# Kernel tuning notes

Measured on AMD Instinct MI355X. Metric: run time of the kernel, lower is better.

Reference implementation:

```python
import jax, jax.numpy as jnp
import numpy as np
import math

EPS = 1e-12  # F.normalize default eps

def _l2_normalize(x):
    n = jnp.sqrt(jnp.sum(x * x, axis=-1, keepdims=True))
    return x / jnp.maximum(n, EPS)

def setup_inputs() -> dict:
    key = jax.random.key(0)
    k1, k2 = jax.random.split(key)
    B, F, C = 16384, 1024, 1000
    features = jax.random.normal(k1, (B, F), dtype=jnp.float32)
    prototypes = jax.random.normal(k2, (C, F), dtype=jnp.float32)
    distance_scale = jnp.ones((1,), dtype=jnp.float32)
    temperature = jnp.ones((1,), dtype=jnp.float32)
    return {"features": features, "prototypes": prototypes,
            "distance_scale": distance_scale, "temperature": temperature}

def reference(features, prototypes, distance_scale, temperature):
    # L2-normalize both sides (F.normalize, p=2, eps=1e-12)
    f = _l2_normalize(features)      # [B, F]
    p = _l2_normalize(prototypes)    # [C, F]
    # Pairwise Euclidean distance. For unit vectors ||f-p||^2 = 2 - 2 f.p,
    # clamped at 0 for numerical safety; then / sqrt(2).
    sim = jnp.einsum('bf,cf->bc', f, p)                  # [B, C]
    sq = jnp.maximum(2.0 - 2.0 * sim, 0.0)
    distances = jnp.sqrt(sq) / jnp.float32(math.sqrt(2.0))
    iso = jnp.abs(distance_scale) * distances            # [B, C]
    logits = -(iso + jnp.mean(iso, axis=1, keepdims=True))
    return logits / temperature
```

## Files before the change

### kernel.cpp

```cpp
#include <hip/hip_runtime.h>
#include <hip/hip_bf16.h>
#include <math.h>

#define B_ROWS 16384
#define C_COLS 1000
#define C_PAD  1024
#define FDIM   1024
#define FBLKS  4096
#define FP8_SCALE 256.0f
#define INV_SIM   (1.0f / (FP8_SCALE * FP8_SCALE))

typedef __attribute__((ext_vector_type(8))) short bf16x8;
typedef __attribute__((ext_vector_type(4))) float f32x4;
typedef __attribute__((ext_vector_type(4))) int   i32x4;
typedef __attribute__((ext_vector_type(8))) int   i32x8;

#define GLD_LDS(gp, lp) __builtin_amdgcn_global_load_lds( \
    (__attribute__((address_space(1))) void*)(gp),        \
    (__attribute__((address_space(3))) void*)(lp), 16, 0, 0)

__global__ __launch_bounds__(256) void normalize_all(
    const float* __restrict__ feat, const float* __restrict__ prot,
    unsigned char* __restrict__ fb, unsigned char* __restrict__ pb,
    float* __restrict__ rowsum)
{
    const int lane = threadIdx.x & 63;
    const int wave = threadIdx.x >> 6;

    if (blockIdx.x < 64) rowsum[blockIdx.x * 256 + threadIdx.x] = 0.0f;

    const float* in;
    unsigned char* out;
    int row, nvalid;
    if (blockIdx.x < FBLKS) {
        row = blockIdx.x * 4 + wave;  in = feat; out = fb; nvalid = B_ROWS;
    } else {
        row = (blockIdx.x - FBLKS) * 4 + wave;  in = prot; out = pb; nvalid = C_COLS;
    }
    unsigned char* orow = out + (size_t)row * FDIM;

    if (row >= nvalid) {
        i32x4 z = {0, 0, 0, 0};
        ((i32x4*)orow)[lane] = z;
        return;
    }

    const float4* rp = (const float4*)(in + (size_t)row * FDIM);
    float4 v[4];
    float ss = 0.0f;
    #pragma unroll
    for (int c = 0; c < 4; ++c) {
        v[c] = rp[lane * 4 + c];
        ss += v[c].x * v[c].x + v[c].y * v[c].y + v[c].z * v[c].z + v[c].w * v[c].w;
    }
    #pragma unroll
    for (int off = 1; off < 64; off <<= 1) ss += __shfl_xor(ss, off, 64);
    const float inv = FP8_SCALE / sqrtf(fmaxf(ss, 1e-24f));

    i32x4 pk;
    #pragma unroll
    for (int c = 0; c < 4; ++c) {
        int w0 = __builtin_amdgcn_cvt_pk_fp8_f32(v[c].x * inv, v[c].y * inv, 0, false);
        w0     = __builtin_amdgcn_cvt_pk_fp8_f32(v[c].z * inv, v[c].w * inv, w0, true);
        pk[c] = w0;
    }
    ((i32x4*)orow)[lane] = pk;
}

__global__ __launch_bounds__(256) void gemm_dist(
    const unsigned char* __restrict__ A,
    const unsigned char* __restrict__ Bp,
    __hip_bfloat16* __restrict__ D,
    float* __restrict__ rowsum)
{
    __shared__ unsigned char As[2 * 128 * 128];
    __shared__ unsigned char Bs[2 * 128 * 128];

    const int tid  = threadIdx.x;
    const int lane = tid & 63;
    const int wave = tid >> 6;

    const int id  = blockIdx.x;
    const int xcd = id & 7;
    const int seq = id >> 3;
    const int bn  = seq & 7;
    const int bm  = xcd * 16 + (seq >> 3);

    const int waveM = (wave >> 1) * 64;
    const int waveN = (wave & 1) * 64;

    f32x4 acc[4][4] = {};

    const int srow8 = lane >> 3;
    const int sg    = (lane & 7) ^ srow8;
    const unsigned char* Abase = A  + ((size_t)(bm * 128 + wave * 8 + srow8)) * FDIM + sg * 16;
    const unsigned char* Bbase = Bp + ((size_t)(bn * 128 + wave * 8 + srow8)) * FDIM + sg * 16;

    const int q2   = (lane >> 4) * 2;
    const int bxor = lane & 7;
    const int fA = (waveM + (lane & 15)) * 128;
    const int fB = (waveN + (lane & 15)) * 128;
    const int pg0 = ((q2)     ^ bxor) * 16;
    const int pg1 = ((q2 + 1) ^ bxor) * 16;

    const int ldsRow = wave * 8 * 128;

    #pragma unroll
    for (int r = 0; r < 4; ++r) {
        GLD_LDS(Abase + (size_t)(r * 32) * FDIM, &As[ldsRow + r * 32 * 128]);
        GLD_LDS(Bbase + (size_t)(r * 32) * FDIM, &Bs[ldsRow + r * 32 * 128]);
    }
    __builtin_amdgcn_sched_barrier(0);
    #pragma unroll
    for (int r = 0; r < 4; ++r) {
        GLD_LDS(Abase + (size_t)(r * 32) * FDIM + 128, &As[16384 + ldsRow + r * 32 * 128]);
        GLD_LDS(Bbase + (size_t)(r * 32) * FDIM + 128, &Bs[16384 + ldsRow + r * 32 * 128]);
    }
    __builtin_amdgcn_sched_barrier(0);

    #pragma unroll 1
    for (int t = 0; t < 7; ++t) {
        asm volatile("s_waitcnt vmcnt(8)" ::: "memory");
        __builtin_amdgcn_s_barrier();
        __builtin_amdgcn_sched_barrier(0);

        const int cur = (t & 1) << 14;

        i32x8 a4[4], b4[4];
        #pragma unroll
        for (int nt = 0; nt < 4; ++nt) {
            const i32x4 lo = *(const i32x4*)&Bs[cur + fB + nt * 2048 + pg0];
            const i32x4 hi = *(const i32x4*)&Bs[cur + fB + nt * 2048 + pg1];
            b4[nt] = (i32x8){lo.x, lo.y, lo.z, lo.w, hi.x, hi.y, hi.z, hi.w};
        }
        #pragma unroll
        for (int mt = 0; mt < 4; ++mt) {
            const i32x4 lo = *(const i32x4*)&As[cur + fA + mt * 2048 + pg0];
            const i32x4 hi = *(const i32x4*)&As[cur + fA + mt * 2048 + pg1];
            a4[mt] = (i32x8){lo.x, lo.y, lo.z, lo.w, hi.x, hi.y, hi.z, hi.w};
        }

        __builtin_amdgcn_s_setprio(1);
        #pragma unroll
        for (int mt = 0; mt < 4; ++mt)
            #pragma unroll
            for (int nt = 0; nt < 4; ++nt)
                acc[mt][nt] = __builtin_amdgcn_mfma_scale_f32_16x16x128_f8f6f4(
                    a4[mt], b4[nt], acc[mt][nt], 0, 0, 0, 127, 0, 127);
        __builtin_amdgcn_s_setprio(0);

        if (t < 6) {
            asm volatile("s_waitcnt lgkmcnt(0)" ::: "memory");
            __builtin_amdgcn_s_barrier();
            __builtin_amdgcn_sched_barrier(0);
            const int k0n = (t + 2) * 128;
            #pragma unroll
            for (int r = 0; r < 4; ++r) {
                GLD_LDS(Abase + (size_t)(r * 32) * FDIM + k0n, &As[cur + ldsRow + r * 32 * 128]);
                GLD_LDS(Bbase + (size_t)(r * 32) * FDIM + k0n, &Bs[cur + ldsRow + r * 32 * 128]);
            }
            __builtin_amdgcn_sched_barrier(0);
        }
    }

    asm volatile("s_waitcnt vmcnt(0)" ::: "memory");
    __builtin_amdgcn_s_barrier();
    __builtin_amdgcn_sched_barrier(0);
    {
        const int cur = 16384;
        i32x8 a4[4], b4[4];
        #pragma unroll
        for (int nt = 0; nt < 4; ++nt) {
            const i32x4 lo = *(const i32x4*)&Bs[cur + fB + nt * 2048 + pg0];
            const i32x4 hi = *(const i32x4*)&Bs[cur + fB + nt * 2048 + pg1];
            b4[nt] = (i32x8){lo.x, lo.y, lo.z, lo.w, hi.x, hi.y, hi.z, hi.w};
        }
        #pragma unroll
        for (int mt = 0; mt < 4; ++mt) {
            const i32x4 lo = *(const i32x4*)&As[cur + fA + mt * 2048 + pg0];
            const i32x4 hi = *(const i32x4*)&As[cur + fA + mt * 2048 + pg1];
            a4[mt] = (i32x8){lo.x, lo.y, lo.z, lo.w, hi.x, hi.y, hi.z, hi.w};
        }
        __builtin_amdgcn_s_setprio(1);
        #pragma unroll
        for (int mt = 0; mt < 4; ++mt)
            #pragma unroll
            for (int nt = 0; nt < 4; ++nt)
                acc[mt][nt] = __builtin_amdgcn_mfma_scale_f32_16x16x128_f8f6f4(
                    a4[mt], b4[nt], acc[mt][nt], 0, 0, 0, 127, 0, 127);
        __builtin_amdgcn_s_setprio(0);
    }

    const int row0 = bm * 128 + waveM;
    const int col0 = bn * 128 + waveN;
    #pragma unroll
    for (int mt = 0; mt < 4; ++mt) {
        #pragma unroll
        for (int r = 0; r < 4; ++r) {
            const int row = row0 + mt * 16 + (lane >> 4) * 4 + r;
            float part = 0.0f;
            #pragma unroll
            for (int nt = 0; nt < 4; ++nt) {
                const int col = col0 + nt * 16 + (lane & 15);
                const float sim = acc[mt][nt][r] * INV_SIM;
                const float dv = sqrtf(fmaxf(1.0f - sim, 0.0f));
                if (col < C_COLS) {
                    D[(size_t)row * C_COLS + col] = __float2bfloat16(dv);
                    part += dv;
                }
            }
            part += __shfl_xor(part, 1, 64);
            part += __shfl_xor(part, 2, 64);
            part += __shfl_xor(part, 4, 64);
            part += __shfl_xor(part, 8, 64);
            if ((lane & 15) == 0) atomicAdd(&rowsum[row], part);
        }
    }
}

__global__ __launch_bounds__(256) void finalize(
    const __hip_bfloat16* __restrict__ D, const float* __restrict__ rowsum,
    const float* __restrict__ scale, const float* __restrict__ temp,
    float* __restrict__ out)
{
    const size_t i = (size_t)blockIdx.x * 256 + threadIdx.x;
    const float a = -fabsf(scale[0]) / temp[0];
    const int row = (int)((i * 8) / C_COLS);
    const float m = rowsum[row] * (1.0f / (float)C_COLS);

    const bf16x8 dv = *(const bf16x8*)(D + i * 8);
    const __hip_bfloat16* dp = (const __hip_bfloat16*)&dv;
    float4 o0, o1;
    o0.x = a * (__bfloat162float(dp[0]) + m);
    o0.y = a * (__bfloat162float(dp[1]) + m);
    o0.z = a * (__bfloat162float(dp[2]) + m);
    o0.w = a * (__bfloat162float(dp[3]) + m);
    o1.x = a * (__bfloat162float(dp[4]) + m);
    o1.y = a * (__bfloat162float(dp[5]) + m);
    o1.z = a * (__bfloat162float(dp[6]) + m);
    o1.w = a * (__bfloat162float(dp[7]) + m);
    ((float4*)out)[i * 2]     = o0;
    ((float4*)out)[i * 2 + 1] = o1;
}

extern "C" void kernel_launch(void* const* d_in, const int* in_sizes, int n_in,
                              void* d_out, int out_size, void* d_ws, size_t ws_size,
                              hipStream_t stream)
{
    const float* features = (const float*)d_in[0];
    const float* protos   = (const float*)d_in[1];
    const float* dscale   = (const float*)d_in[2];
    const float* temp     = (const float*)d_in[3];
    float* out = (float*)d_out;

    char* ws = (char*)d_ws;
    unsigned char* fb = (unsigned char*)ws;
    unsigned char* pb = (unsigned char*)(ws + 16777216);
    __hip_bfloat16* D = (__hip_bfloat16*)(ws + 17825792);
    float* rowsum     = (float*)(ws + 50593792);

    normalize_all<<<FBLKS + C_PAD / 4, 256, 0, stream>>>(features, protos, fb, pb, rowsum);

    gemm_dist<<<1024, 256, 0, stream>>>(fb, pb, D, rowsum);

    finalize<<<(B_ROWS * C_COLS / 8) / 256, 256, 0, stream>>>(D, rowsum, dscale, temp, out);
}
```

Before: 159.2 us.

## Fuse finalize into GEMM via per-row-band last-block completion counter

Result: slower. 235.1 us (+47.7%).

```diff
diff --git a/kernel.cpp b/kernel.cpp
--- a/kernel.cpp
+++ b/kernel.cpp
@@ -22,12 +22,13 @@
 __global__ __launch_bounds__(256) void normalize_all(
     const float* __restrict__ feat, const float* __restrict__ prot,
     unsigned char* __restrict__ fb, unsigned char* __restrict__ pb,
-    float* __restrict__ rowsum)
+    float* __restrict__ rowsum, unsigned int* __restrict__ cnt)
 {
     const int lane = threadIdx.x & 63;
     const int wave = threadIdx.x >> 6;
 
     if (blockIdx.x < 64) rowsum[blockIdx.x * 256 + threadIdx.x] = 0.0f;
+    if (blockIdx.x == 64 && threadIdx.x < 128) cnt[threadIdx.x] = 0u;
 
     const float* in;
     unsigned char* out;
@@ -71,10 +72,15 @@
     const unsigned char* __restrict__ A,
     const unsigned char* __restrict__ Bp,
     __hip_bfloat16* __restrict__ D,
-    float* __restrict__ rowsum)
+    float* __restrict__ rowsum,
+    unsigned int* __restrict__ cnt,
+    const float* __restrict__ scale,
+    const float* __restrict__ temp,
+    float* __restrict__ out)
 {
     __shared__ unsigned char As[2 * 128 * 128];
     __shared__ unsigned char Bs[2 * 128 * 128];
+    __shared__ int last_flag;
 
     const int tid  = threadIdx.x;
     const int lane = tid & 63;
@@ -216,31 +222,39 @@
             if ((lane & 15) == 0) atomicAdd(&rowsum[row], part);
         }
     }
-}
-
-__global__ __launch_bounds__(256) void finalize(
-    const __hip_bfloat16* __restrict__ D, const float* __restrict__ rowsum,
-    const float* __restrict__ scale, const float* __restrict__ temp,
-    float* __restrict__ out)
-{
-    const size_t i = (size_t)blockIdx.x * 256 + threadIdx.x;
-    const float a = -fabsf(scale[0]) / temp[0];
-    const int row = (int)((i * 8) / C_COLS);
-    const float m = rowsum[row] * (1.0f / (float)C_COLS);
-
-    const bf16x8 dv = *(const bf16x8*)(D + i * 8);
-    const __hip_bfloat16* dp = (const __hip_bfloat16*)&dv;
-    float4 o0, o1;
-    o0.x = a * (__bfloat162float(dp[0]) + m);
-    o0.y = a * (__bfloat162float(dp[1]) + m);
-    o0.z = a * (__bfloat162float(dp[2]) + m);
-    o0.w = a * (__bfloat162float(dp[3]) + m);
-    o1.x = a * (__bfloat162float(dp[4]) + m);
-    o1.y = a * (__bfloat162float(dp[5]) + m);
-    o1.z = a * (__bfloat162float(dp[6]) + m);
-    o1.w = a * (__bfloat162float(dp[7]) + m);
-    ((float4*)out)[i * 2]     = o0;
-    ((float4*)out)[i * 2 + 1] = o1;
+
+    __syncthreads();
+    if (tid == 0) {
+        unsigned int old = __hip_atomic_fetch_add(&cnt[bm], 1u,
+                                                  __ATOMIC_ACQ_REL, __HIP_MEMORY_SCOPE_AGENT);
+        last_flag = (old == 7u);
+    }
+    __syncthreads();
+
+    if (last_flag) {
+        const float aS = -fabsf(scale[0]) / temp[0];
+        const int rbase = bm * 128;
+        for (int g = tid; g < 16000; g += 256) {
+            const int rloc = g / 125;
+            const int row  = rbase + rloc;
+            const float m = __hip_atomic_load(&rowsum[row], __ATOMIC_RELAXED,
+                                              __HIP_MEMORY_SCOPE_AGENT) * (1.0f / (float)C_COLS);
+            const size_t idx = (size_t)row * C_COLS + (g - rloc * 125) * 8;
+            const bf16x8 dv = *(const bf16x8*)(D + idx);
+            const __hip_bfloat16* dp = (const __hip_bfloat16*)&dv;
+            float4 o0, o1;
+            o0.x = aS * (__bfloat162float(dp[0]) + m);
+            o0.y = aS * (__bfloat162float(dp[1]) + m);
+            o0.z = aS * (__bfloat162float(dp[2]) + m);
+            o0.w = aS * (__bfloat162float(dp[3]) + m);
+            o1.x = aS * (__bfloat162float(dp[4]) + m);
+            o1.y = aS * (__bfloat162float(dp[5]) + m);
+            o1.z = aS * (__bfloat162float(dp[6]) + m);
+            o1.w = aS * (__bfloat162float(dp[7]) + m);
+            *(float4*)(out + idx)     = o0;
+            *(float4*)(out + idx + 4) = o1;
+        }
+    }
 }
 
 extern "C" void kernel_launch(void* const* d_in, const int* in_sizes, int n_in,
@@ -258,10 +272,9 @@
     unsigned char* pb = (unsigned char*)(ws + 16777216);
     __hip_bfloat16* D = (__hip_bfloat16*)(ws + 17825792);
     float* rowsum     = (float*)(ws + 50593792);
-
-    normalize_all<<<FBLKS + C_PAD / 4, 256, 0, stream>>>(features, protos, fb, pb, rowsum);
-
-    gemm_dist<<<1024, 256, 0, stream>>>(fb, pb, D, rowsum);
-
-    finalize<<<(B_ROWS * C_COLS / 8) / 256, 256, 0, stream>>>(D, rowsum, dscale, temp, out);
+    unsigned int* cnt = (unsigned int*)(ws + 50659328);
+
+    normalize_all<<<FBLKS + C_PAD / 4, 256, 0, stream>>>(features, protos, fb, pb, rowsum, cnt);
+
+    gemm_dist<<<1024, 256, 0, stream>>>(fb, pb, D, rowsum, cnt, dscale, temp, out);
 }
```

## Load A fragments directly from global memory, stage only B through LDS

Applied to the files above, without the earlier changes.

Result: slower. 174.8 us (+9.8%).

```diff
diff --git a/kernel.cpp b/kernel.cpp
--- a/kernel.cpp
+++ b/kernel.cpp
@@ -73,7 +73,6 @@
     __hip_bfloat16* __restrict__ D,
     float* __restrict__ rowsum)
 {
-    __shared__ unsigned char As[2 * 128 * 128];
     __shared__ unsigned char Bs[2 * 128 * 128];
 
     const int tid  = threadIdx.x;
@@ -93,51 +92,62 @@
 
     const int srow8 = lane >> 3;
     const int sg    = (lane & 7) ^ srow8;
-    const unsigned char* Abase = A  + ((size_t)(bm * 128 + wave * 8 + srow8)) * FDIM + sg * 16;
     const unsigned char* Bbase = Bp + ((size_t)(bn * 128 + wave * 8 + srow8)) * FDIM + sg * 16;
 
     const int q2   = (lane >> 4) * 2;
     const int bxor = lane & 7;
-    const int fA = (waveM + (lane & 15)) * 128;
     const int fB = (waveN + (lane & 15)) * 128;
     const int pg0 = ((q2)     ^ bxor) * 16;
     const int pg1 = ((q2 + 1) ^ bxor) * 16;
 
+    const unsigned char* Afrag =
+        A + ((size_t)(bm * 128 + waveM + (lane & 15))) * FDIM + (lane >> 4) * 32;
+
     const int ldsRow = wave * 8 * 128;
 
     #pragma unroll
-    for (int r = 0; r < 4; ++r) {
-        GLD_LDS(Abase + (size_t)(r * 32) * FDIM, &As[ldsRow + r * 32 * 128]);
+    for (int r = 0; r < 4; ++r)
         GLD_LDS(Bbase + (size_t)(r * 32) * FDIM, &Bs[ldsRow + r * 32 * 128]);
-    }
     __builtin_amdgcn_sched_barrier(0);
     #pragma unroll
-    for (int r = 0; r < 4; ++r) {
-        GLD_LDS(Abase + (size_t)(r * 32) * FDIM + 128, &As[16384 + ldsRow + r * 32 * 128]);
+    for (int r = 0; r < 4; ++r)
         GLD_LDS(Bbase + (size_t)(r * 32) * FDIM + 128, &Bs[16384 + ldsRow + r * 32 * 128]);
-    }
     __builtin_amdgcn_sched_barrier(0);
 
     #pragma unroll 1
     for (int t = 0; t < 7; ++t) {
-        asm volatile("s_waitcnt vmcnt(8)" ::: "memory");
+        asm volatile("s_waitcnt vmcnt(4)" ::: "memory");
         __builtin_amdgcn_s_barrier();
         __builtin_amdgcn_sched_barrier(0);
 
         const int cur = (t & 1) << 14;
-
-        i32x8 a4[4], b4[4];
+        const int k0  = t * 128;
+
+        i32x8 a4[4];
+        #pragma unroll
+        for (int mt = 0; mt < 4; ++mt) {
+            const i32x4 lo = *(const i32x4*)(Afrag + (size_t)mt * 16 * FDIM + k0);
+            const i32x4 hi = *(const i32x4*)(Afrag + (size_t)mt * 16 * FDIM + k0 + 16);
+            a4[mt] = (i32x8){lo.x, lo.y, lo.z, lo.w, hi.x, hi.y, hi.z, hi.w};
+        }
+
+        i32x8 b4[4];
         #pragma unroll
         for (int nt = 0; nt < 4; ++nt) {
             const i32x4 lo = *(const i32x4*)&Bs[cur + fB + nt * 2048 + pg0];
             const i32x4 hi = *(const i32x4*)&Bs[cur + fB + nt * 2048 + pg1];
             b4[nt] = (i32x8){lo.x, lo.y, lo.z, lo.w, hi.x, hi.y, hi.z, hi.w};
         }
-        #pragma unroll
-        for (int mt = 0; mt < 4; ++mt) {
-            const i32x4 lo = *(const i32x4*)&As[cur + fA + mt * 2048 + pg0];
-            const i32x4 hi = *(const i32x4*)&As[cur + fA + mt * 2048 + pg1];
-            a4[mt] = (i32x8){lo.x, lo.y, lo.z, lo.w, hi.x, hi.y, hi.z, hi.w};
+
+        asm volatile("s_waitcnt lgkmcnt(0)" ::: "memory");
+        __builtin_amdgcn_s_barrier();
+        __builtin_amdgcn_sched_barrier(0);
+        if (t < 6) {
+            const int k0n = (t + 2) * 128;
+            #pragma unroll
+            for (int r = 0; r < 4; ++r)
+                GLD_LDS(Bbase + (size_t)(r * 32) * FDIM + k0n, &Bs[cur + ldsRow + r * 32 * 128]);
+            __builtin_amdgcn_sched_barrier(0);
         }
 
         __builtin_amdgcn_s_setprio(1);
@@ -148,19 +158,6 @@
                 acc[mt][nt] = __builtin_amdgcn_mfma_scale_f32_16x16x128_f8f6f4(
                     a4[mt], b4[nt], acc[mt][nt], 0, 0, 0, 127, 0, 127);
         __builtin_amdgcn_s_setprio(0);
-
-        if (t < 6) {
-            asm volatile("s_waitcnt lgkmcnt(0)" ::: "memory");
-            __builtin_amdgcn_s_barrier();
-            __builtin_amdgcn_sched_barrier(0);
-            const int k0n = (t + 2) * 128;
-            #pragma unroll
-            for (int r = 0; r < 4; ++r) {
-                GLD_LDS(Abase + (size_t)(r * 32) * FDIM + k0n, &As[cur + ldsRow + r * 32 * 128]);
-                GLD_LDS(Bbase + (size_t)(r * 32) * FDIM + k0n, &Bs[cur + ldsRow + r * 32 * 128]);
-            }
-            __builtin_amdgcn_sched_barrier(0);
-        }
     }
 
     asm volatile("s_waitcnt vmcnt(0)" ::: "memory");
@@ -168,18 +165,19 @@
     __builtin_amdgcn_sched_barrier(0);
     {
         const int cur = 16384;
+        const int k0  = 7 * 128;
         i32x8 a4[4], b4[4];
+        #pragma unroll
+        for (int mt = 0; mt < 4; ++mt) {
+            const i32x4 lo = *(const i32x4*)(Afrag + (size_t)mt * 16 * FDIM + k0);
+            const i32x4 hi = *(const i32x4*)(Afrag + (size_t)mt * 16 * FDIM + k0 + 16);
+            a4[mt] = (i32x8){lo.x, lo.y, lo.z, lo.w, hi.x, hi.y, hi.z, hi.w};
+        }
         #pragma unroll
         for (int nt = 0; nt < 4; ++nt) {
             const i32x4 lo = *(const i32x4*)&Bs[cur + fB + nt * 2048 + pg0];
             const i32x4 hi = *(const i32x4*)&Bs[cur + fB + nt * 2048 + pg1];
             b4[nt] = (i32x8){lo.x, lo.y, lo.z, lo.w, hi.x, hi.y, hi.z, hi.w};
-        }
-        #pragma unroll
-        for (int mt = 0; mt < 4; ++mt) {
-            const i32x4 lo = *(const i32x4*)&As[cur + fA + mt * 2048 + pg0];
-            const i32x4 hi = *(const i32x4*)&As[cur + fA + mt * 2048 + pg1];
-            a4[mt] = (i32x8){lo.x, lo.y, lo.z, lo.w, hi.x, hi.y, hi.z, hi.w};
         }
         __builtin_amdgcn_s_setprio(1);
         #pragma unroll
```
